# Kernel optimization log

Hardware: AMD Instinct MI355X
Metric: run time of the kernel (lower is better)

The kernel has to match this reference:

```python
import jax, jax.numpy as jnp
import numpy as np

N_HEAD = 8
D_HEAD = 64
D_MODEL = 512
CTX = 64
B = 2
Q_LEN = 2048
T = Q_LEN + CTX - 1


def setup_inputs() -> dict:
    key = jax.random.key(0)
    ks = jax.random.split(key, 7)
    HD = N_HEAD * D_HEAD
    return {
        "x": jax.random.normal(ks[0], (B, T, D_MODEL), jnp.float32),
        "r": jax.random.normal(ks[1], (CTX, D_MODEL), jnp.float32),
        "Wkv": jax.random.normal(ks[2], (D_MODEL, 2 * HD), jnp.float32) * 0.02,
        "Wq": jax.random.normal(ks[3], (D_MODEL, HD), jnp.float32) * 0.02,
        "bq": jax.random.normal(ks[4], (HD,), jnp.float32) * 0.02,
        "Wr": jax.random.normal(ks[5], (D_MODEL, HD), jnp.float32) * 0.02,
        "Wo": jax.random.normal(ks[6], (HD, D_MODEL), jnp.float32) * 0.02,
    }


def reference(x, r, Wkv, Wq, bq, Wr, Wo):
    Bb, Tt, _ = x.shape
    C = r.shape[0]
    H, Dh = N_HEAD, D_HEAD
    q_len = Tt - C + 1
    scale = Dh ** -0.5

    kv = x @ Wkv                                  # [B, T, 2*H*Dh]
    k_all = kv[..., : H * Dh].reshape(Bb, Tt, H, Dh)
    v_all = kv[..., H * Dh:].reshape(Bb, Tt, H, Dh)

    # sliding windows (torch unfold(1, ctx, 1) equivalent)
    idx = jnp.arange(q_len)[:, None] + jnp.arange(C)[None, :]   # [q, C]
    k_win = k_all[:, idx]                         # [B, q, C, H, Dh]
    v_win = v_all[:, idx]                         # [B, q, C, H, Dh]

    hq = (x[:, C - 1:] @ Wq + bq).reshape(Bb, q_len, H, Dh)     # [B, q, H, Dh]
    hr = (r @ Wr).reshape(C, H, Dh)                              # [C, H, Dh]

    # q . (k + r): split into content term + relative-position bias term
    scores = (jnp.einsum('bqhd,bqchd->bhqc', hq, k_win)
              + jnp.einsum('bqhd,chd->bhqc', hq, hr)) * scale    # [B, H, q, C]

    # padding mask: positions in first ctx-1 steps that are all-zero
    pad_mask = jnp.all(x[:, : C - 1] == 0, axis=-1)              # [B, C-1]
    full_mask = jnp.concatenate(
        [pad_mask, jnp.zeros((Bb, q_len), dtype=bool)], axis=1)  # [B, T]
    mask_win = full_mask[:, idx]                                 # [B, q, C]
    scores = jnp.where(mask_win[:, None], -jnp.inf, scores)

    w = jax.nn.softmax(scores, axis=-1)                          # [B, H, q, C]
    out = jnp.einsum('bhqc,bqchd->bqhd', w, v_win).reshape(Bb, q_len, H * Dh)
    return out @ Wo                                              # [B, q, d_model]
```

## Files before the change

### kernel.cpp

```cpp
#include <hip/hip_runtime.h>
#include <cstdint>
#include <cstddef>

#define NH 8
#define DH 64
#define DM 512
#define CTX 64
#define BB 2
#define QL 2048
#define TT (QL + CTX - 1)
#define HDIM 512
#define KVN 1024
#define KD 512

typedef unsigned short u16;
typedef __attribute__((ext_vector_type(8))) short bf16x8;
typedef __attribute__((ext_vector_type(4))) float f32x4;

__device__ __forceinline__ u16 f2bf(float f) {
    uint32_t u = __float_as_uint(f);
    u += 0x7FFF + ((u >> 16) & 1);
    return (u16)(u >> 16);
}

#define GLLDS(g, l) __builtin_amdgcn_global_load_lds( \
    (const __attribute__((address_space(1))) void*)(g), \
    (__attribute__((address_space(3))) void*)(l), 16, 0, 0)

struct Ptrs {
    const float *x, *r, *Wkv, *Wq, *bq, *Wr, *Wo;
    float* outp;
    u16 *xb, *WkvqT, *WoT, *kvb, *hqb, *hrb, *attnb;
    float* maskv;
};

__global__ __launch_bounds__(256) void k_prep(Ptrs p)
{
    __shared__ __align__(16) char smem[16648];
    int bid = blockIdx.x;
    const int tid = threadIdx.x;

    if (bid < 2111) {
        int i = bid * 256 + tid;
        float4 v = ((const float4*)p.x)[i];
        ushort4 o; o.x = f2bf(v.x); o.y = f2bf(v.y); o.z = f2bf(v.z); o.w = f2bf(v.w);
        ((ushort4*)p.xb)[i] = o;
        return;
    }
    bid -= 2111;

    if (bid < 256) {
        float (*tile)[65] = (float(*)[65])smem;
        const float* W; u16* WT; int N; int tidx;
        if (bid < 128)      { W = p.Wkv; WT = p.WkvqT;                      N = 1024; tidx = bid; }
        else if (bid < 192) { W = p.Wq;  WT = p.WkvqT + (size_t)1024 * 512; N = 512;  tidx = bid - 128; }
        else                { W = p.Wo;  WT = p.WoT;                        N = 512;  tidx = bid - 192; }
        const int tpr = N / 64;
        const int kb = (tidx / tpr) * 64, nbo = (tidx % tpr) * 64;
        const int c4 = (tid & 15) * 4;
        for (int kk = tid >> 4; kk < 64; kk += 16) {
            float4 v = *(const float4*)&W[(size_t)(kb + kk) * N + nbo + c4];
            tile[kk][c4 + 0] = v.x; tile[kk][c4 + 1] = v.y;
            tile[kk][c4 + 2] = v.z; tile[kk][c4 + 3] = v.w;
        }
        __syncthreads();
        for (int nn = tid >> 4; nn < 64; nn += 16) {
            ushort4 o;
            o.x = f2bf(tile[c4 + 0][nn]); o.y = f2bf(tile[c4 + 1][nn]);
            o.z = f2bf(tile[c4 + 2][nn]); o.w = f2bf(tile[c4 + 3][nn]);
            *(ushort4*)&WT[(size_t)(nbo + nn) * KD + kb + c4] = o;
        }
        return;
    }
    bid -= 256;

    if (bid < 8) {
        float (*As)[68] = (float(*)[68])smem;
        float (*Bs)[68] = (float(*)[68])(smem + 4352);
        const int tx = tid & 15, ty = tid >> 4;
        const int n0 = bid * 64;
        const int mloc = tid >> 2;
        const int ka4  = (tid & 3) * 4;
        const float* aptr = p.r + (size_t)mloc * KD + ka4;
        const int kb  = tid >> 4;
        const int nb4 = (tid & 15) * 4;
        const float* bptr = p.Wr + (size_t)kb * DM + n0 + nb4;

        float acc[4][4] = {};
        for (int kt = 0; kt < KD; kt += 16) {
            float4 av = *(const float4*)(aptr + kt);
            float4 bv = *(const float4*)(bptr + (size_t)kt * DM);
            __syncthreads();
            As[ka4 + 0][mloc] = av.x; As[ka4 + 1][mloc] = av.y;
            As[ka4 + 2][mloc] = av.z; As[ka4 + 3][mloc] = av.w;
            *(float4*)&Bs[kb][nb4] = bv;
            __syncthreads();
#pragma unroll
            for (int kk = 0; kk < 16; kk++) {
                float4 a = *(const float4*)&As[kk][ty * 4];
                float4 b = *(const float4*)&Bs[kk][tx * 4];
                acc[0][0] += a.x * b.x; acc[0][1] += a.x * b.y; acc[0][2] += a.x * b.z; acc[0][3] += a.x * b.w;
                acc[1][0] += a.y * b.x; acc[1][1] += a.y * b.y; acc[1][2] += a.y * b.z; acc[1][3] += a.y * b.w;
                acc[2][0] += a.z * b.x; acc[2][1] += a.z * b.y; acc[2][2] += a.z * b.z; acc[2][3] += a.z * b.w;
                acc[3][0] += a.w * b.x; acc[3][1] += a.w * b.y; acc[3][2] += a.w * b.z; acc[3][3] += a.w * b.w;
            }
        }
#pragma unroll
        for (int i = 0; i < 4; i++) {
            int m = ty * 4 + i;
            ushort4 o;
            o.x = f2bf(acc[i][0]); o.y = f2bf(acc[i][1]);
            o.z = f2bf(acc[i][2]); o.w = f2bf(acc[i][3]);
            *(ushort4*)&p.hrb[(size_t)m * HDIM + n0 + tx * 4] = o;
        }
        return;
    }
    bid -= 8;

    {
        int* anyflag = (int*)smem;
        int t = bid >> 1, b = bid & 1;
        const float* row = p.x + (size_t)(b * TT + t) * DM;
        bool nz = (row[tid] != 0.f) || (row[tid + 256] != 0.f);
        if (tid == 0) *anyflag = 0;
        __syncthreads();
        unsigned long long bal = __ballot(nz);
        if ((tid & 63) == 0 && bal) atomicOr(anyflag, 1);
        __syncthreads();
        if (tid == 0) p.maskv[b * 64 + t] = *anyflag ? 0.f : -1e30f;
    }
}

__global__ __launch_bounds__(256) void k_g1(Ptrs p)
{
    __shared__ u16 As[128 * 32];
    __shared__ u16 Bs[128 * 32];

    const int tid  = threadIdx.x;
    const int lane = tid & 63;
    const int w    = tid >> 6;
    const int wm   = (w >> 1) * 64;
    const int wn   = (w & 1) * 64;
    const int m0   = blockIdx.y * 128;
    const int n0   = blockIdx.x * 128;

    const u16* ga0 = p.xb    + (size_t)(m0 + (tid >> 2)) * KD + (tid & 3) * 8;
    const u16* ga1 = ga0 + (size_t)64 * KD;
    const u16* gb0 = p.WkvqT + (size_t)(n0 + (tid >> 2)) * KD + (tid & 3) * 8;
    const u16* gb1 = gb0 + (size_t)64 * KD;

    f32x4 acc[4][4];
#pragma unroll
    for (int i = 0; i < 4; i++)
#pragma unroll
        for (int j = 0; j < 4; j++)
            acc[i][j] = (f32x4){0.f, 0.f, 0.f, 0.f};

    const int fm = lane & 15;
    const int fk = (lane >> 4) * 8;

    for (int kt = 0; kt < KD; kt += 32) {
        __syncthreads();
        GLLDS(ga0 + kt, &As[w * 512]);
        GLLDS(ga1 + kt, &As[2048 + w * 512]);
        GLLDS(gb0 + kt, &Bs[w * 512]);
        GLLDS(gb1 + kt, &Bs[2048 + w * 512]);
        __syncthreads();

        bf16x8 af[4], bfr[4];
#pragma unroll
        for (int i = 0; i < 4; i++)
            af[i] = *(const bf16x8*)&As[(wm + i * 16 + fm) * 32 + fk];
#pragma unroll
        for (int j = 0; j < 4; j++)
            bfr[j] = *(const bf16x8*)&Bs[(wn + j * 16 + fm) * 32 + fk];
#pragma unroll
        for (int i = 0; i < 4; i++)
#pragma unroll
            for (int j = 0; j < 4; j++)
                acc[i][j] = __builtin_amdgcn_mfma_f32_16x16x32_bf16(af[i], bfr[j], acc[i][j], 0, 0, 0);
    }

    const int fc = lane & 15;
    const int fr = (lane >> 4) * 4;
    const bool iskv = (n0 < 1024);
#pragma unroll
    for (int i = 0; i < 4; i++)
#pragma unroll
        for (int rr = 0; rr < 4; rr++) {
            int row = m0 + wm + i * 16 + fr + rr;
            if (row < BB * TT) {
                if (iskv) {
#pragma unroll
                    for (int j = 0; j < 4; j++) {
                        int col = n0 + wn + j * 16 + fc;
                        p.kvb[(size_t)row * KVN + col] = f2bf(acc[i][j][rr]);
                    }
                } else {
                    int bb = row / TT;
                    int t  = row - bb * TT;
                    if (t >= CTX - 1) {
                        size_t orow = (size_t)(bb * QL + t - (CTX - 1));
#pragma unroll
                        for (int j = 0; j < 4; j++) {
                            int col = n0 + wn + j * 16 + fc - 1024;
                            p.hqb[orow * HDIM + col] = f2bf(acc[i][j][rr] + p.bq[col]);
                        }
                    }
                }
            }
        }
}

__global__ __launch_bounds__(256) void k_g2(Ptrs p)
{
    __shared__ u16 As[128 * 32];
    __shared__ u16 Bs[64 * 32];

    const int tid  = threadIdx.x;
    const int lane = tid & 63;
    const int w    = tid >> 6;
    const int wm   = (w >> 1) * 64;
    const int wn   = (w & 1) * 32;
    const int m0   = (blockIdx.x >> 3) * 128;
    const int n0   = (blockIdx.x & 7) * 64;

    const u16* ga0 = p.attnb + (size_t)(m0 + (tid >> 2)) * KD + (tid & 3) * 8;
    const u16* ga1 = ga0 + (size_t)64 * KD;
    const u16* gb0 = p.WoT + (size_t)(n0 + (tid >> 2)) * KD + (tid & 3) * 8;

    f32x4 acc[4][2];
#pragma unroll
    for (int i = 0; i < 4; i++)
#pragma unroll
        for (int j = 0; j < 2; j++)
            acc[i][j] = (f32x4){0.f, 0.f, 0.f, 0.f};

    const int fm = lane & 15;
    const int fk = (lane >> 4) * 8;

    for (int kt = 0; kt < KD; kt += 32) {
        __syncthreads();
        GLLDS(ga0 + kt, &As[w * 512]);
        GLLDS(ga1 + kt, &As[2048 + w * 512]);
        GLLDS(gb0 + kt, &Bs[w * 512]);
        __syncthreads();

        bf16x8 af[4], bfr[2];
#pragma unroll
        for (int i = 0; i < 4; i++)
            af[i] = *(const bf16x8*)&As[(wm + i * 16 + fm) * 32 + fk];
#pragma unroll
        for (int j = 0; j < 2; j++)
            bfr[j] = *(const bf16x8*)&Bs[(wn + j * 16 + fm) * 32 + fk];
#pragma unroll
        for (int i = 0; i < 4; i++)
#pragma unroll
            for (int j = 0; j < 2; j++)
                acc[i][j] = __builtin_amdgcn_mfma_f32_16x16x32_bf16(af[i], bfr[j], acc[i][j], 0, 0, 0);
    }

    const int fc = lane & 15;
    const int fr = (lane >> 4) * 4;
#pragma unroll
    for (int i = 0; i < 4; i++)
#pragma unroll
        for (int rr = 0; rr < 4; rr++) {
            int row = m0 + wm + i * 16 + fr + rr;
#pragma unroll
            for (int j = 0; j < 2; j++) {
                int col = n0 + wn + j * 16 + fc;
                p.outp[(size_t)row * DM + col] = acc[i][j][rr];
            }
        }
}

__global__ __launch_bounds__(256, 2) void k_attn(Ptrs p)
{
    __shared__ __align__(16) char smem[55296];
    float* sprime = (float*)smem;
    u16*   vTs    = (u16*)smem;
    float* s2s    = (float*)(smem + 20480);
    u16*   wband  = (u16*)(smem + 37888);

    const int u = blockIdx.x;
    const int q0 = (u & 31) * 64;
    const int h  = (u >> 5) & 7;
    const int b  = u >> 8;
    const int tid  = threadIdx.x;
    const int lane = tid & 63;
    const int w    = tid >> 6;
    const int qb   = q0 + w * 16;

    {
        uint32_t* wz = (uint32_t*)wband;
#pragma unroll
        for (int i = 0; i < 17; i++) wz[tid + i * 256] = 0;
    }
    __syncthreads();

    const int fm = lane & 15;
    const int fk = (lane >> 4) * 8;

    const u16* hqrow = p.hqb + (size_t)(b * QL + qb + fm) * HDIM + h * DH + fk;
    bf16x8 afr0 = *(const bf16x8*)(hqrow);
    bf16x8 afr1 = *(const bf16x8*)(hqrow + 32);

    {
        const u16* kbase = p.kvb + (size_t)(b * TT + qb + fm) * KVN + h * DH + fk;
#pragma unroll
        for (int nt = 0; nt < 5; nt++) {
            bf16x8 b0 = *(const bf16x8*)(kbase + (size_t)nt * 16 * KVN);
            bf16x8 b1 = *(const bf16x8*)(kbase + (size_t)nt * 16 * KVN + 32);
            f32x4 acc = (f32x4){0.f, 0.f, 0.f, 0.f};
            acc = __builtin_amdgcn_mfma_f32_16x16x32_bf16(afr0, b0, acc, 0, 0, 0);
            acc = __builtin_amdgcn_mfma_f32_16x16x32_bf16(afr1, b1, acc, 0, 0, 0);
            const int row = (lane >> 4) * 4;
#pragma unroll
            for (int rr = 0; rr < 4; rr++)
                sprime[w * 1280 + (row + rr) * 80 + nt * 16 + fm] = acc[rr];
        }
    }
    {
        const u16* hrbase = p.hrb + (size_t)fm * HDIM + h * DH + fk;
#pragma unroll
        for (int nc = 0; nc < 4; nc++) {
            bf16x8 b0 = *(const bf16x8*)(hrbase + (size_t)nc * 16 * HDIM);
            bf16x8 b1 = *(const bf16x8*)(hrbase + (size_t)nc * 16 * HDIM + 32);
            f32x4 acc = (f32x4){0.f, 0.f, 0.f, 0.f};
            acc = __builtin_amdgcn_mfma_f32_16x16x32_bf16(afr0, b0, acc, 0, 0, 0);
            acc = __builtin_amdgcn_mfma_f32_16x16x32_bf16(afr1, b1, acc, 0, 0, 0);
            const int row = (lane >> 4) * 4;
#pragma unroll
            for (int rr = 0; rr < 4; rr++)
                s2s[w * 1088 + (row + rr) * 68 + nc * 16 + fm] = acc[rr];
        }
    }

#pragma unroll 1
    for (int i = 0; i < 16; i++) {
        const int qloc = w * 16 + i;
        float s = (sprime[w * 1280 + i * 80 + i + lane] +
                   s2s[w * 1088 + i * 68 + lane]) * 0.125f;
        if (q0 == 0) {
            int t = qloc + lane;
            if (t < 63) s += p.maskv[b * 64 + t];
        }
        float mx = s;
#pragma unroll
        for (int off = 32; off; off >>= 1) mx = fmaxf(mx, __shfl_xor(mx, off, 64));
        float e = __expf(s - mx);
        float sum = e;
#pragma unroll
        for (int off = 32; off; off >>= 1) sum += __shfl_xor(sum, off, 64);
        wband[qloc * 136 + qloc + lane] = f2bf(e / sum);
    }
    __syncthreads();

    {
        const int r0 = tid >> 4;
        const int c4 = (tid & 15) * 4;
        for (int rr = r0; rr < 127; rr += 16) {
            ushort4 vv = *(const ushort4*)&p.kvb[(size_t)(b * TT + q0 + rr) * KVN + HDIM + h * DH + c4];
            vTs[(c4 + 0) * 136 + rr] = vv.x;
            vTs[(c4 + 1) * 136 + rr] = vv.y;
            vTs[(c4 + 2) * 136 + rr] = vv.z;
            vTs[(c4 + 3) * 136 + rr] = vv.w;
        }
        if (tid < 64) vTs[tid * 136 + 127] = 0;
    }
    __syncthreads();

    f32x4 oacc[4];
#pragma unroll
    for (int j = 0; j < 4; j++) oacc[j] = (f32x4){0.f, 0.f, 0.f, 0.f};
#pragma unroll
    for (int ks = 0; ks < 4; ks++) {
        bf16x8 wa = *(const bf16x8*)&wband[(w * 16 + fm) * 136 + ks * 32 + fk];
#pragma unroll
        for (int j = 0; j < 4; j++) {
            bf16x8 vb = *(const bf16x8*)&vTs[(j * 16 + fm) * 136 + ks * 32 + fk];
            oacc[j] = __builtin_amdgcn_mfma_f32_16x16x32_bf16(wa, vb, oacc[j], 0, 0, 0);
        }
    }
    {
        const int row = (lane >> 4) * 4;
#pragma unroll
        for (int j = 0; j < 4; j++)
#pragma unroll
            for (int rr = 0; rr < 4; rr++)
                p.attnb[(size_t)(b * QL + qb + row + rr) * HDIM + h * DH + j * 16 + fm] =
                    f2bf(oacc[j][rr]);
    }
}

extern "C" void kernel_launch(void* const* d_in, const int* in_sizes, int n_in,
                              void* d_out, int out_size, void* d_ws, size_t ws_size,
                              hipStream_t stream)
{
    Ptrs p;
    p.x   = (const float*)d_in[0];
    p.r   = (const float*)d_in[1];
    p.Wkv = (const float*)d_in[2];
    p.Wq  = (const float*)d_in[3];
    p.bq  = (const float*)d_in[4];
    p.Wr  = (const float*)d_in[5];
    p.Wo  = (const float*)d_in[6];
    p.outp = (float*)d_out;

    char* w = (char*)d_ws;
    p.xb    = (u16*)w;  w += (size_t)4224 * 512 * 2;
    p.WkvqT = (u16*)w;  w += (size_t)1536 * 512 * 2;
    p.WoT   = (u16*)w;  w += (size_t)512 * 512 * 2;
    p.kvb   = (u16*)w;  w += (size_t)4224 * 1024 * 2;
    p.hqb   = (u16*)w;  w += (size_t)4096 * 512 * 2;
    p.hrb   = (u16*)w;  w += (size_t)64 * 512 * 2;
    p.attnb = (u16*)w;  w += (size_t)4096 * 512 * 2;
    p.maskv = (float*)w;

    hipLaunchKernelGGL(k_prep, dim3(2501),   dim3(256), 0, stream, p);
    hipLaunchKernelGGL(k_g1,   dim3(12, 33), dim3(256), 0, stream, p);
    hipLaunchKernelGGL(k_attn, dim3(512),    dim3(256), 0, stream, p);
    hipLaunchKernelGGL(k_g2,   dim3(256),    dim3(256), 0, stream, p);
}
```

Before: 146.2 us.

## Alias attention LDS buffers to raise occupancy and split hr projection across blocks

The attention kernel's shared memory drops from 55 KB to about 37 KB by overlaying the softmax weight band on the relative-position score buffer. Each row is read before it is overwritten, and the band is now zeroed per row inside the softmax loop instead of in a separate up-front pass with an extra barrier. Launch bounds go from 2 to 4 blocks per CU so more blocks can be resident. Separately, the small r@Wr projection in the prep kernel is spread over 32 blocks of 16 columns instead of 8 blocks of 64, which shortens that tail at the cost of scalar loads. The aliasing depends on the row strides of both buffers matching exactly, and the higher occupancy target may limit registers.

```diff
diff --git a/kernel.cpp b/kernel.cpp
--- a/kernel.cpp
+++ b/kernel.cpp
@@ -74,48 +74,40 @@
     }
     bid -= 256;
 
-    if (bid < 8) {
+    if (bid < 32) {
         float (*As)[68] = (float(*)[68])smem;
-        float (*Bs)[68] = (float(*)[68])(smem + 4352);
-        const int tx = tid & 15, ty = tid >> 4;
-        const int n0 = bid * 64;
+        float (*Bs)[20] = (float(*)[20])(smem + 4352);
+        const int tx = tid & 15;
+        const int ty = tid >> 4;
+        const int n0 = bid * 16;
         const int mloc = tid >> 2;
         const int ka4  = (tid & 3) * 4;
         const float* aptr = p.r + (size_t)mloc * KD + ka4;
-        const int kb  = tid >> 4;
-        const int nb4 = (tid & 15) * 4;
-        const float* bptr = p.Wr + (size_t)kb * DM + n0 + nb4;
-
-        float acc[4][4] = {};
+        const float* bptr = p.Wr + (size_t)ty * DM + n0 + tx;
+
+        float acc[4] = {};
         for (int kt = 0; kt < KD; kt += 16) {
             float4 av = *(const float4*)(aptr + kt);
-            float4 bv = *(const float4*)(bptr + (size_t)kt * DM);
+            float  bv = bptr[(size_t)kt * DM];
             __syncthreads();
             As[ka4 + 0][mloc] = av.x; As[ka4 + 1][mloc] = av.y;
             As[ka4 + 2][mloc] = av.z; As[ka4 + 3][mloc] = av.w;
-            *(float4*)&Bs[kb][nb4] = bv;
+            Bs[ty][tx] = bv;
             __syncthreads();
 #pragma unroll
             for (int kk = 0; kk < 16; kk++) {
                 float4 a = *(const float4*)&As[kk][ty * 4];
-                float4 b = *(const float4*)&Bs[kk][tx * 4];
-                acc[0][0] += a.x * b.x; acc[0][1] += a.x * b.y; acc[0][2] += a.x * b.z; acc[0][3] += a.x * b.w;
-                acc[1][0] += a.y * b.x; acc[1][1] += a.y * b.y; acc[1][2] += a.y * b.z; acc[1][3] += a.y * b.w;
-                acc[2][0] += a.z * b.x; acc[2][1] += a.z * b.y; acc[2][2] += a.z * b.z; acc[2][3] += a.z * b.w;
-                acc[3][0] += a.w * b.x; acc[3][1] += a.w * b.y; acc[3][2] += a.w * b.z; acc[3][3] += a.w * b.w;
+                float  b = Bs[kk][tx];
+                acc[0] += a.x * b; acc[1] += a.y * b;
+                acc[2] += a.z * b; acc[3] += a.w * b;
             }
         }
 #pragma unroll
-        for (int i = 0; i < 4; i++) {
-            int m = ty * 4 + i;
-            ushort4 o;
-            o.x = f2bf(acc[i][0]); o.y = f2bf(acc[i][1]);
-            o.z = f2bf(acc[i][2]); o.w = f2bf(acc[i][3]);
-            *(ushort4*)&p.hrb[(size_t)m * HDIM + n0 + tx * 4] = o;
-        }
+        for (int i = 0; i < 4; i++)
+            p.hrb[(size_t)(ty * 4 + i) * HDIM + n0 + tx] = f2bf(acc[i]);
         return;
     }
-    bid -= 8;
+    bid -= 32;
 
     {
         int* anyflag = (int*)smem;
@@ -275,13 +267,13 @@
         }
 }
 
-__global__ __launch_bounds__(256, 2) void k_attn(Ptrs p)
+__global__ __launch_bounds__(256, 4) void k_attn(Ptrs p)
 {
-    __shared__ __align__(16) char smem[55296];
+    __shared__ __align__(16) char smem[37888];
     float* sprime = (float*)smem;
     u16*   vTs    = (u16*)smem;
-    float* s2s    = (float*)(smem + 20480);
-    u16*   wband  = (u16*)(smem + 37888);
+    float* s2u    = (float*)(smem + 20480);
+    u16*   wband  = (u16*)(smem + 20480);
 
     const int u = blockIdx.x;
     const int q0 = (u & 31) * 64;
@@ -292,13 +284,6 @@
     const int w    = tid >> 6;
     const int qb   = q0 + w * 16;
 
-    {
-        uint32_t* wz = (uint32_t*)wband;
-#pragma unroll
-        for (int i = 0; i < 17; i++) wz[tid + i * 256] = 0;
-    }
-    __syncthreads();
-
     const int fm = lane & 15;
     const int fk = (lane >> 4) * 8;
 
@@ -333,7 +318,7 @@
             const int row = (lane >> 4) * 4;
 #pragma unroll
             for (int rr = 0; rr < 4; rr++)
-                s2s[w * 1088 + (row + rr) * 68 + nc * 16 + fm] = acc[rr];
+                s2u[(size_t)(w * 16 + row + rr) * 68 + nc * 16 + fm] = acc[rr];
         }
     }
 
@@ -341,7 +326,7 @@
     for (int i = 0; i < 16; i++) {
         const int qloc = w * 16 + i;
         float s = (sprime[w * 1280 + i * 80 + i + lane] +
-                   s2s[w * 1088 + i * 68 + lane]) * 0.125f;
+                   s2u[(size_t)qloc * 68 + lane]) * 0.125f;
         if (q0 == 0) {
             int t = qloc + lane;
             if (t < 63) s += p.maskv[b * 64 + t];
@@ -354,6 +339,10 @@
 #pragma unroll
         for (int off = 32; off; off >>= 1) sum += __shfl_xor(sum, off, 64);
         wband[qloc * 136 + qloc + lane] = f2bf(e / sum);
+        if (lane < 72) {
+            int z = (lane < qloc) ? lane : lane + 64;
+            wband[qloc * 136 + z] = 0;
+        }
     }
     __syncthreads();
 
@@ -418,7 +407,7 @@
     p.attnb = (u16*)w;  w += (size_t)4096 * 512 * 2;
     p.maskv = (float*)w;
 
-    hipLaunchKernelGGL(k_prep, dim3(2501),   dim3(256), 0, stream, p);
+    hipLaunchKernelGGL(k_prep, dim3(2525),   dim3(256), 0, stream, p);
     hipLaunchKernelGGL(k_g1,   dim3(12, 33), dim3(256), 0, stream, p);
     hipLaunchKernelGGL(k_attn, dim3(512),    dim3(256), 0, stream, p);
     hipLaunchKernelGGL(k_g2,   dim3(256),    dim3(256), 0, stream, p);
```

Result: faster. 143.2 us (-2.0%).
